# Performance work log

Hardware: AMD Instinct MI355X
Metric: run time of the kernel (lower is better)

## Reference

```python
import jax, jax.numpy as jnp
import numpy as np

# Model dims (match init_kwargs)
H = 2048          # hidden_size
I = 1408          # moe_intermediate_size
E = 16            # n_routed_experts
K = 2             # num_experts_per_tok
N_SHARED = 2      # n_shared_experts -> shared intermediate = I * N_SHARED
IS = I * N_SHARED
ROUTED_SCALE = 1.0
# Expert capacity for the static dispatch buffer. Mean load = T*K/E = 512;
CAPACITY = 1024


def setup_inputs() -> dict:
    key = jax.random.key(0)
    ks = jax.random.split(key, 8)
    B, S = 2, 1024
    scale = 0.02
    return {
        "hidden_states": jax.random.normal(ks[0], (B, S, H), jnp.float32),
        "gate_w": jax.random.normal(ks[1], (E, H), jnp.float32) * scale,      # router logits weight
        "w_gate": jax.random.normal(ks[2], (E, H, I), jnp.float32) * scale,   # expert gate_proj
        "w_up": jax.random.normal(ks[3], (E, H, I), jnp.float32) * scale,     # expert up_proj
        "w_down": jax.random.normal(ks[4], (E, I, H), jnp.float32) * scale,   # expert down_proj
        "ws_gate": jax.random.normal(ks[5], (H, IS), jnp.float32) * scale,    # shared gate_proj
        "ws_up": jax.random.normal(ks[6], (H, IS), jnp.float32) * scale,      # shared up_proj
        "ws_down": jax.random.normal(ks[7], (IS, H), jnp.float32) * scale,    # shared down_proj
    }


def _moe_forward(hidden_states, gate_w, w_gate, w_up, w_down, ws_gate, ws_up, ws_down):
    B, S, _ = hidden_states.shape
    x = hidden_states.reshape(-1, H)                      # [T, H]
    T = x.shape[0]

    # ---- MoEGate: softmax scores, greedy top-k (no renorm, scale=1.0) ----
    logits = jnp.einsum('th,eh->te', x.astype(jnp.float32), gate_w.astype(jnp.float32))
    scores = jax.nn.softmax(logits, axis=-1)              # [T, E]
    topk_w, topk_idx = jax.lax.top_k(scores, K)           # [T, K]
    topk_w = (topk_w * ROUTED_SCALE).astype(x.dtype)

    # ---- dispatch: sort token-assignments by expert (argsort + gather) ----
    flat_idx = topk_idx.reshape(-1)                       # [T*K]
    order = jnp.argsort(flat_idx)                         # stable sort by expert id
    sorted_e = flat_idx[order]                            # expert id per sorted slot
    sorted_t = order // K                                 # source token per sorted slot
    counts = jnp.bincount(flat_idx, length=E)             # tokens per expert
    starts = jnp.cumsum(counts) - counts                  # exclusive prefix sum
    pos = jnp.arange(T * K) - starts[sorted_e]            # slot within its expert group

    # [E, CAPACITY, H] buffer; pos < CAPACITY always holds at this scale
    buf = jnp.zeros((E, CAPACITY, H), x.dtype).at[sorted_e, pos].set(x[sorted_t], mode='drop')

    # ---- per-expert SwiGLU MLP as batched GEMMs over the expert dim ----
    g = jax.nn.silu(jnp.einsum('ech,ehi->eci', buf, w_gate))
    u = jnp.einsum('ech,ehi->eci', buf, w_up)
    expert_out = jnp.einsum('eci,eih->ech', g * u, w_down)  # [E, C, H]

    # ---- combine: gather back, unpermute, weighted sum over k ----
    gathered = expert_out[sorted_e, pos]                  # [T*K, H] in sorted order
    out_flat = jnp.zeros((T * K, H), x.dtype).at[order].set(gathered)
    y = (out_flat.reshape(T, K, H) * topk_w[..., None]).sum(axis=1)  # [T, H]

    # ---- shared experts on the identity path ----
    sh = jnp.einsum('ti,ih->th', jax.nn.silu(x @ ws_gate) * (x @ ws_up), ws_down)
    return (y + sh).reshape(B, S, H)


def reference(hidden_states, gate_w, w_gate, w_up, w_down, ws_gate, ws_up, ws_down):
    return _moe_forward(hidden_states, gate_w, w_gate, w_up, w_down, ws_gate, ws_up, ws_down)
```

## Files before the change

### kernel.cpp

```cpp
#include <hip/hip_runtime.h>
#include <hip/hip_bf16.h>
#include <stdint.h>
#include <math.h>

#define H_DIM 2048
#define I_DIM 1408
#define E_NUM 16
#define IS_DIM 2816
#define T_NUM 2048
#define A_NUM 4096

typedef float f32x4 __attribute__((ext_vector_type(4)));
typedef __bf16 bf16x8 __attribute__((ext_vector_type(8)));
typedef __bf16 bf16x4 __attribute__((ext_vector_type(4)));

__device__ __forceinline__ void async16(const __bf16* g, __bf16* l) {
  __builtin_amdgcn_global_load_lds((__attribute__((address_space(1))) void*)g,
                                   (__attribute__((address_space(3))) void*)l,
                                   16, 0, 0);
}

__global__ __launch_bounds__(256) void k_convert_x(const float* __restrict__ x,
                                                   __bf16* __restrict__ xb) {
  int i = (blockIdx.x * 256 + threadIdx.x) * 4;
  float4 v = *(const float4*)(x + i);
  bf16x4 o;
  o[0] = (__bf16)v.x; o[1] = (__bf16)v.y; o[2] = (__bf16)v.z; o[3] = (__bf16)v.w;
  *(bf16x4*)(xb + i) = o;
}

__global__ __launch_bounds__(256) void k_router(const float* __restrict__ x,
                                                const float* __restrict__ gw,
                                                int* __restrict__ tki,
                                                float* __restrict__ tkw) {
  __shared__ float red[E_NUM * 256];
  __shared__ float st[256];
  __shared__ float sc[E_NUM];
  int t = blockIdx.x, tid = threadIdx.x;
  const float* xr = x + (size_t)t * H_DIM + tid * 8;
  float4 xv0 = *(const float4*)xr;
  float4 xv1 = *(const float4*)(xr + 4);
#pragma unroll
  for (int e = 0; e < E_NUM; e++) {
    const float* g = gw + e * H_DIM + tid * 8;
    float4 a = *(const float4*)g;
    float4 b = *(const float4*)(g + 4);
    red[e * 256 + tid] = xv0.x * a.x + xv0.y * a.y + xv0.z * a.z + xv0.w * a.w +
                         xv1.x * b.x + xv1.y * b.y + xv1.z * b.z + xv1.w * b.w;
  }
  __syncthreads();
  {
    int e = tid >> 4, j = tid & 15;
    float s = 0.f;
#pragma unroll
    for (int m = 0; m < 16; m++) s += red[e * 256 + m * 16 + j];
    st[e * 16 + j] = s;
  }
  __syncthreads();
  if (tid < E_NUM) {
    float s = 0.f;
#pragma unroll
    for (int m = 0; m < 16; m++) s += st[tid * 16 + m];
    sc[tid] = s;
  }
  __syncthreads();
  if (tid == 0) {
    int i1 = 0;
    for (int q = 1; q < E_NUM; q++) if (sc[q] > sc[i1]) i1 = q;
    int i2 = (i1 == 0) ? 1 : 0;
    for (int q = 0; q < E_NUM; q++) if (q != i1 && sc[q] > sc[i2]) i2 = q;
    float mx = sc[i1], Z = 0.f;
    for (int q = 0; q < E_NUM; q++) Z += expf(sc[q] - mx);
    tki[t * 2] = i1;
    tki[t * 2 + 1] = i2;
    tkw[t * 2] = 1.0f / Z;
    tkw[t * 2 + 1] = expf(sc[i2] - mx) / Z;
  }
}

__global__ __launch_bounds__(256) void k_count(const int* __restrict__ tki,
                                               int* __restrict__ grp,
                                               int* __restrict__ cur,
                                               int* __restrict__ grps,
                                               __bf16* __restrict__ zb) {
  __shared__ int cnt[E_NUM];
  int tid = threadIdx.x;
  if (tid < E_NUM) cnt[tid] = 0;
  __syncthreads();
  for (int i = tid; i < A_NUM; i += 256) atomicAdd(&cnt[tki[i]], 1);
  __syncthreads();
  if (tid == 0) {
    int off = 0;
    for (int e = 0; e < E_NUM; e++) { grp[e] = off; cur[e] = off; off += cnt[e]; }
    grp[E_NUM] = off;
    grps[0] = 0; grps[1] = T_NUM;
  }
  if (tid < 64) zb[tid] = (__bf16)0.f;
}

__global__ __launch_bounds__(256) void k_fill(const int* __restrict__ tki,
                                              int* __restrict__ cur,
                                              int* __restrict__ slot_of,
                                              int* __restrict__ tok_of) {
  int i = blockIdx.x * 256 + threadIdx.x;
  if (i < A_NUM) {
    int e = tki[i];
    int s = atomicAdd(&cur[e], 1);
    slot_of[i] = s;
    tok_of[s] = i >> 1;
  }
}

__global__ __launch_bounds__(256) void k_gather(const __bf16* __restrict__ xb,
                                                const int* __restrict__ tok_of,
                                                __bf16* __restrict__ buf) {
  int gid = blockIdx.x * 256 + threadIdx.x;
  int s = gid >> 8;
  int off = (gid & 255) * 8;
  int t = tok_of[s];
  *(uint4*)(buf + (size_t)s * H_DIM + off) = *(const uint4*)(xb + (size_t)t * H_DIM + off);
}

__global__ __launch_bounds__(256) void k_transpose(const float* __restrict__ in,
                                                   __bf16* __restrict__ out,
                                                   int R, int C) {
  __shared__ float tile[32][33];
  size_t zb = (size_t)blockIdx.z * R * C;
  int c0 = blockIdx.x * 32, r0 = blockIdx.y * 32;
  int x = threadIdx.x, y = threadIdx.y;
#pragma unroll
  for (int i = 0; i < 4; i++)
    tile[y + 8 * i][x] = in[zb + (size_t)(r0 + y + 8 * i) * C + c0 + x];
  __syncthreads();
#pragma unroll
  for (int i = 0; i < 4; i++)
    out[zb + (size_t)(c0 + y + 8 * i) * R + r0 + x] = (__bf16)tile[x][y + 8 * i];
}

__global__ __launch_bounds__(256) void k_gemm(const __bf16* __restrict__ A,
                                              const __bf16* __restrict__ Bt,
                                              __bf16* __restrict__ C,
                                              const int* __restrict__ grp,
                                              const __bf16* __restrict__ zb,
                                              int K, int N) {
  int g = blockIdx.z;
  int mstart = grp[g], mend = grp[g + 1];
  int m0 = mstart + blockIdx.y * 128;
  if (m0 >= mend) return;
  int n0 = blockIdx.x * 128;
  const __bf16* Bg = Bt + (size_t)g * N * K;

  __shared__ __align__(16) __bf16 As[128 * 32];
  __shared__ __align__(16) __bf16 Bs[128 * 32];

  int tid = threadIdx.x;
  int wave = tid >> 6, lane = tid & 63;
  int srow = wave * 16 + (lane >> 2);
  int scol = (lane & 3) * 8;

  int rA1 = m0 + srow, rA2 = m0 + srow + 64;
  bool okA1 = rA1 < mend, okA2 = rA2 < mend;
  const __bf16* baseA1 = A + (size_t)rA1 * K + scol;
  const __bf16* baseA2 = A + (size_t)rA2 * K + scol;
  const __bf16* baseB1 = Bg + (size_t)(n0 + srow) * K + scol;
  const __bf16* baseB2 = Bg + (size_t)(n0 + srow + 64) * K + scol;

  __bf16* ldsA1 = As + wave * 512;
  __bf16* ldsA2 = As + 2048 + wave * 512;
  __bf16* ldsB1 = Bs + wave * 512;
  __bf16* ldsB2 = Bs + 2048 + wave * 512;

  int wm = (wave >> 1) * 64, wn = (wave & 1) * 64;
  int r16 = lane & 15, quad = lane >> 4;

  f32x4 acc[4][4] = {};
  for (int k0 = 0; k0 < K; k0 += 32) {
    __syncthreads();
    async16(okA1 ? baseA1 + k0 : zb, ldsA1);
    async16(okA2 ? baseA2 + k0 : zb, ldsA2);
    async16(baseB1 + k0, ldsB1);
    async16(baseB2 + k0, ldsB2);
    __syncthreads();
    bf16x8 af[4], bq[4];
#pragma unroll
    for (int i = 0; i < 4; i++)
      af[i] = *(const bf16x8*)(As + (wm + i * 16 + r16) * 32 + quad * 8);
#pragma unroll
    for (int i = 0; i < 4; i++)
      bq[i] = *(const bf16x8*)(Bs + (wn + i * 16 + r16) * 32 + quad * 8);
#pragma unroll
    for (int mi = 0; mi < 4; mi++)
#pragma unroll
      for (int ni = 0; ni < 4; ni++)
        acc[mi][ni] = __builtin_amdgcn_mfma_f32_16x16x32_bf16(af[mi], bq[ni],
                                                              acc[mi][ni], 0, 0, 0);
  }
#pragma unroll
  for (int mi = 0; mi < 4; mi++) {
    int row_base = m0 + wm + mi * 16 + quad * 4;
#pragma unroll
    for (int r = 0; r < 4; r++) {
      int row = row_base + r;
      if (row < mend) {
#pragma unroll
        for (int ni = 0; ni < 4; ni++) {
          int col = n0 + wn + ni * 16 + r16;
          C[(size_t)row * N + col] = (__bf16)acc[mi][ni][r];
        }
      }
    }
  }
}

__global__ __launch_bounds__(256) void k_silu_mul(const __bf16* __restrict__ G,
                                                  const __bf16* __restrict__ U,
                                                  __bf16* __restrict__ M) {
  int i = (blockIdx.x * 256 + threadIdx.x) * 4;
  bf16x4 g = *(const bf16x4*)(G + i);
  bf16x4 u = *(const bf16x4*)(U + i);
  bf16x4 o;
#pragma unroll
  for (int j = 0; j < 4; j++) {
    float gv = (float)g[j], uv = (float)u[j];
    float s = gv / (1.f + expf(-gv));
    o[j] = (__bf16)(s * uv);
  }
  *(bf16x4*)(M + i) = o;
}

__global__ __launch_bounds__(256) void k_combine(const __bf16* __restrict__ SH,
                                                 const __bf16* __restrict__ EO,
                                                 const int* __restrict__ slot_of,
                                                 const float* __restrict__ tkw,
                                                 float* __restrict__ out) {
  int gid = blockIdx.x * 256 + threadIdx.x;
  int t = gid >> 9;
  int c = (gid & 511) * 4;
  int s1 = slot_of[t * 2], s2 = slot_of[t * 2 + 1];
  float w1 = tkw[t * 2], w2 = tkw[t * 2 + 1];
  bf16x4 sh = *(const bf16x4*)(SH + (size_t)t * H_DIM + c);
  bf16x4 e1 = *(const bf16x4*)(EO + (size_t)s1 * H_DIM + c);
  bf16x4 e2 = *(const bf16x4*)(EO + (size_t)s2 * H_DIM + c);
  float4 o;
  o.x = (float)sh[0] + w1 * (float)e1[0] + w2 * (float)e2[0];
  o.y = (float)sh[1] + w1 * (float)e1[1] + w2 * (float)e2[1];
  o.z = (float)sh[2] + w1 * (float)e1[2] + w2 * (float)e2[2];
  o.w = (float)sh[3] + w1 * (float)e1[3] + w2 * (float)e2[3];
  *(float4*)(out + (size_t)t * H_DIM + c) = o;
}

extern "C" void kernel_launch(void* const* d_in, const int* in_sizes, int n_in,
                              void* d_out, int out_size, void* d_ws, size_t ws_size,
                              hipStream_t stream) {
  const float* x       = (const float*)d_in[0];
  const float* gate_w  = (const float*)d_in[1];
  const float* w_gate  = (const float*)d_in[2];
  const float* w_up    = (const float*)d_in[3];
  const float* w_down  = (const float*)d_in[4];
  const float* ws_gate = (const float*)d_in[5];
  const float* ws_up   = (const float*)d_in[6];
  const float* ws_down = (const float*)d_in[7];
  float* out = (float*)d_out;

  char* p = (char*)d_ws;
  auto alloc = [&](size_t bytes) {
    char* r = p;
    p += (bytes + 255) & ~(size_t)255;
    return r;
  };
  __bf16* WT   = (__bf16*)alloc((size_t)E_NUM * H_DIM * I_DIM * 2);
  __bf16* XB   = (__bf16*)alloc((size_t)T_NUM * H_DIM * 2);
  __bf16* BUF  = (__bf16*)alloc((size_t)A_NUM * H_DIM * 2);
  __bf16* G    = (__bf16*)alloc((size_t)A_NUM * I_DIM * 2);
  __bf16* U    = (__bf16*)alloc((size_t)A_NUM * I_DIM * 2);
  __bf16* M    = (__bf16*)alloc((size_t)A_NUM * I_DIM * 2);
  __bf16* EO   = (__bf16*)alloc((size_t)A_NUM * H_DIM * 2);
  __bf16* SH   = (__bf16*)alloc((size_t)T_NUM * H_DIM * 2);
  int* TKI     = (int*)alloc(A_NUM * 4);
  float* TKW   = (float*)alloc(A_NUM * 4);
  int* GRP     = (int*)alloc(128);
  int* GRPS    = (int*)alloc(128);
  int* CUR     = (int*)alloc(128);
  int* SLOT    = (int*)alloc(A_NUM * 4);
  int* TOK     = (int*)alloc(A_NUM * 4);
  __bf16* ZB   = (__bf16*)alloc(256);
  if ((size_t)(p - (char*)d_ws) > ws_size) return;

  k_convert_x<<<4096, 256, 0, stream>>>(x, XB);
  k_router<<<2048, 256, 0, stream>>>(x, gate_w, TKI, TKW);
  k_count<<<1, 256, 0, stream>>>(TKI, GRP, CUR, GRPS, ZB);
  k_fill<<<16, 256, 0, stream>>>(TKI, CUR, SLOT, TOK);
  k_gather<<<4096, 256, 0, stream>>>(XB, TOK, BUF);

  k_transpose<<<dim3(44, 64, 16), dim3(32, 8), 0, stream>>>(w_gate, WT, 2048, 1408);
  k_gemm<<<dim3(11, 8, 16), 256, 0, stream>>>(BUF, WT, G, GRP, ZB, 2048, 1408);
  k_transpose<<<dim3(44, 64, 16), dim3(32, 8), 0, stream>>>(w_up, WT, 2048, 1408);
  k_gemm<<<dim3(11, 8, 16), 256, 0, stream>>>(BUF, WT, U, GRP, ZB, 2048, 1408);
  k_silu_mul<<<5632, 256, 0, stream>>>(G, U, M);
  k_transpose<<<dim3(64, 44, 16), dim3(32, 8), 0, stream>>>(w_down, WT, 1408, 2048);
  k_gemm<<<dim3(16, 8, 16), 256, 0, stream>>>(M, WT, EO, GRP, ZB, 1408, 2048);

  k_transpose<<<dim3(88, 64, 1), dim3(32, 8), 0, stream>>>(ws_gate, WT, 2048, 2816);
  k_gemm<<<dim3(22, 16, 1), 256, 0, stream>>>(XB, WT, G, GRPS, ZB, 2048, 2816);
  k_transpose<<<dim3(88, 64, 1), dim3(32, 8), 0, stream>>>(ws_up, WT, 2048, 2816);
  k_gemm<<<dim3(22, 16, 1), 256, 0, stream>>>(XB, WT, U, GRPS, ZB, 2048, 2816);
  k_silu_mul<<<5632, 256, 0, stream>>>(G, U, M);
  k_transpose<<<dim3(64, 88, 1), dim3(32, 8), 0, stream>>>(ws_down, WT, 2816, 2048);
  k_gemm<<<dim3(16, 16, 1), 256, 0, stream>>>(M, WT, SH, GRPS, ZB, 2816, 2048);

  k_combine<<<4096, 256, 0, stream>>>(SH, EO, SLOT, TKW, out);
}
```

Before: 1.034 ms.

## Fuse gate/up GEMMs with SiLU epilogue, merge dispatch kernels, enlarge transpose tiles

Gate and up projections are computed in one GEMM kernel that shares the A tile and applies SiLU·up in the epilogue, so the separate G/U buffers and the silu_mul kernel go away. The count and fill kernels are merged into a single dispatch kernel that uses shared-memory atomics. Weight transposes now use 64x64 tiles with a 64x4 thread block. The down GEMM uses 128x64 tiles to give more blocks. Together these cut launches and intermediate HBM traffic, but each block now does less work per A load for the down GEMM, and the transposes use a larger LDS footprint.

```diff
diff --git a/kernel.cpp b/kernel.cpp
--- a/kernel.cpp
+++ b/kernel.cpp
@@ -18,6 +18,10 @@
   __builtin_amdgcn_global_load_lds((__attribute__((address_space(1))) void*)g,
                                    (__attribute__((address_space(3))) void*)l,
                                    16, 0, 0);
+}
+
+__device__ __forceinline__ float silu_f(float g) {
+  return g / (1.f + __expf(-g));
 }
 
 __global__ __launch_bounds__(256) void k_convert_x(const float* __restrict__ x,
@@ -78,12 +82,14 @@
   }
 }
 
-__global__ __launch_bounds__(256) void k_count(const int* __restrict__ tki,
-                                               int* __restrict__ grp,
-                                               int* __restrict__ cur,
-                                               int* __restrict__ grps,
-                                               __bf16* __restrict__ zb) {
+__global__ __launch_bounds__(256) void k_dispatch(const int* __restrict__ tki,
+                                                  int* __restrict__ grp,
+                                                  int* __restrict__ grps,
+                                                  int* __restrict__ slot_of,
+                                                  int* __restrict__ tok_of,
+                                                  __bf16* __restrict__ zb) {
   __shared__ int cnt[E_NUM];
+  __shared__ int cur[E_NUM];
   int tid = threadIdx.x;
   if (tid < E_NUM) cnt[tid] = 0;
   __syncthreads();
@@ -96,14 +102,8 @@
     grps[0] = 0; grps[1] = T_NUM;
   }
   if (tid < 64) zb[tid] = (__bf16)0.f;
-}
-
-__global__ __launch_bounds__(256) void k_fill(const int* __restrict__ tki,
-                                              int* __restrict__ cur,
-                                              int* __restrict__ slot_of,
-                                              int* __restrict__ tok_of) {
-  int i = blockIdx.x * 256 + threadIdx.x;
-  if (i < A_NUM) {
+  __syncthreads();
+  for (int i = tid; i < A_NUM; i += 256) {
     int e = tki[i];
     int s = atomicAdd(&cur[e], 1);
     slot_of[i] = s;
@@ -124,34 +124,37 @@
 __global__ __launch_bounds__(256) void k_transpose(const float* __restrict__ in,
                                                    __bf16* __restrict__ out,
                                                    int R, int C) {
-  __shared__ float tile[32][33];
+  __shared__ float tile[64][65];
   size_t zb = (size_t)blockIdx.z * R * C;
-  int c0 = blockIdx.x * 32, r0 = blockIdx.y * 32;
+  int c0 = blockIdx.x * 64, r0 = blockIdx.y * 64;
   int x = threadIdx.x, y = threadIdx.y;
 #pragma unroll
-  for (int i = 0; i < 4; i++)
-    tile[y + 8 * i][x] = in[zb + (size_t)(r0 + y + 8 * i) * C + c0 + x];
-  __syncthreads();
-#pragma unroll
-  for (int i = 0; i < 4; i++)
-    out[zb + (size_t)(c0 + y + 8 * i) * R + r0 + x] = (__bf16)tile[x][y + 8 * i];
-}
-
-__global__ __launch_bounds__(256) void k_gemm(const __bf16* __restrict__ A,
-                                              const __bf16* __restrict__ Bt,
-                                              __bf16* __restrict__ C,
-                                              const int* __restrict__ grp,
-                                              const __bf16* __restrict__ zb,
-                                              int K, int N) {
+  for (int i = 0; i < 16; i++)
+    tile[y + 4 * i][x] = in[zb + (size_t)(r0 + y + 4 * i) * C + c0 + x];
+  __syncthreads();
+#pragma unroll
+  for (int i = 0; i < 16; i++)
+    out[zb + (size_t)(c0 + y + 4 * i) * R + r0 + x] = (__bf16)tile[x][y + 4 * i];
+}
+
+__global__ __launch_bounds__(256) void k_gemm_gu(const __bf16* __restrict__ A,
+                                                 const __bf16* __restrict__ Bg,
+                                                 const __bf16* __restrict__ Bu,
+                                                 __bf16* __restrict__ Mb,
+                                                 const int* __restrict__ grp,
+                                                 const __bf16* __restrict__ zb,
+                                                 int K, int N) {
   int g = blockIdx.z;
   int mstart = grp[g], mend = grp[g + 1];
   int m0 = mstart + blockIdx.y * 128;
   if (m0 >= mend) return;
-  int n0 = blockIdx.x * 128;
-  const __bf16* Bg = Bt + (size_t)g * N * K;
+  int n0 = blockIdx.x * 64;
+  const __bf16* Bgg = Bg + (size_t)g * N * K;
+  const __bf16* Bug = Bu + (size_t)g * N * K;
 
   __shared__ __align__(16) __bf16 As[128 * 32];
-  __shared__ __align__(16) __bf16 Bs[128 * 32];
+  __shared__ __align__(16) __bf16 Gs[64 * 32];
+  __shared__ __align__(16) __bf16 Us[64 * 32];
 
   int tid = threadIdx.x;
   int wave = tid >> 6, lane = tid & 63;
@@ -162,38 +165,43 @@
   bool okA1 = rA1 < mend, okA2 = rA2 < mend;
   const __bf16* baseA1 = A + (size_t)rA1 * K + scol;
   const __bf16* baseA2 = A + (size_t)rA2 * K + scol;
-  const __bf16* baseB1 = Bg + (size_t)(n0 + srow) * K + scol;
-  const __bf16* baseB2 = Bg + (size_t)(n0 + srow + 64) * K + scol;
+  const __bf16* baseG = Bgg + (size_t)(n0 + srow) * K + scol;
+  const __bf16* baseU = Bug + (size_t)(n0 + srow) * K + scol;
 
   __bf16* ldsA1 = As + wave * 512;
   __bf16* ldsA2 = As + 2048 + wave * 512;
-  __bf16* ldsB1 = Bs + wave * 512;
-  __bf16* ldsB2 = Bs + 2048 + wave * 512;
-
-  int wm = (wave >> 1) * 64, wn = (wave & 1) * 64;
+  __bf16* ldsG = Gs + wave * 512;
+  __bf16* ldsU = Us + wave * 512;
+
+  int wm = (wave >> 1) * 64, wn = (wave & 1) * 32;
   int r16 = lane & 15, quad = lane >> 4;
 
-  f32x4 acc[4][4] = {};
+  f32x4 accg[4][2] = {}, accu[4][2] = {};
   for (int k0 = 0; k0 < K; k0 += 32) {
     __syncthreads();
     async16(okA1 ? baseA1 + k0 : zb, ldsA1);
     async16(okA2 ? baseA2 + k0 : zb, ldsA2);
-    async16(baseB1 + k0, ldsB1);
-    async16(baseB2 + k0, ldsB2);
+    async16(baseG + k0, ldsG);
+    async16(baseU + k0, ldsU);
     __syncthreads();
-    bf16x8 af[4], bq[4];
+    bf16x8 af[4], bg[2], bu[2];
 #pragma unroll
     for (int i = 0; i < 4; i++)
       af[i] = *(const bf16x8*)(As + (wm + i * 16 + r16) * 32 + quad * 8);
 #pragma unroll
-    for (int i = 0; i < 4; i++)
-      bq[i] = *(const bf16x8*)(Bs + (wn + i * 16 + r16) * 32 + quad * 8);
+    for (int i = 0; i < 2; i++) {
+      bg[i] = *(const bf16x8*)(Gs + (wn + i * 16 + r16) * 32 + quad * 8);
+      bu[i] = *(const bf16x8*)(Us + (wn + i * 16 + r16) * 32 + quad * 8);
+    }
 #pragma unroll
     for (int mi = 0; mi < 4; mi++)
 #pragma unroll
-      for (int ni = 0; ni < 4; ni++)
-        acc[mi][ni] = __builtin_amdgcn_mfma_f32_16x16x32_bf16(af[mi], bq[ni],
-                                                              acc[mi][ni], 0, 0, 0);
+      for (int ni = 0; ni < 2; ni++) {
+        accg[mi][ni] = __builtin_amdgcn_mfma_f32_16x16x32_bf16(af[mi], bg[ni],
+                                                               accg[mi][ni], 0, 0, 0);
+        accu[mi][ni] = __builtin_amdgcn_mfma_f32_16x16x32_bf16(af[mi], bu[ni],
+                                                               accu[mi][ni], 0, 0, 0);
+      }
   }
 #pragma unroll
   for (int mi = 0; mi < 4; mi++) {
@@ -203,29 +211,86 @@
       int row = row_base + r;
       if (row < mend) {
 #pragma unroll
-        for (int ni = 0; ni < 4; ni++) {
+        for (int ni = 0; ni < 2; ni++) {
+          int col = n0 + wn + ni * 16 + r16;
+          float v = silu_f(accg[mi][ni][r]) * accu[mi][ni][r];
+          Mb[(size_t)row * N + col] = (__bf16)v;
+        }
+      }
+    }
+  }
+}
+
+__global__ __launch_bounds__(256) void k_gemm_dn(const __bf16* __restrict__ A,
+                                                 const __bf16* __restrict__ Bt,
+                                                 __bf16* __restrict__ C,
+                                                 const int* __restrict__ grp,
+                                                 const __bf16* __restrict__ zb,
+                                                 int K, int N) {
+  int g = blockIdx.z;
+  int mstart = grp[g], mend = grp[g + 1];
+  int m0 = mstart + blockIdx.y * 128;
+  if (m0 >= mend) return;
+  int n0 = blockIdx.x * 64;
+  const __bf16* Bg = Bt + (size_t)g * N * K;
+
+  __shared__ __align__(16) __bf16 As[128 * 32];
+  __shared__ __align__(16) __bf16 Bs[64 * 32];
+
+  int tid = threadIdx.x;
+  int wave = tid >> 6, lane = tid & 63;
+  int srow = wave * 16 + (lane >> 2);
+  int scol = (lane & 3) * 8;
+
+  int rA1 = m0 + srow, rA2 = m0 + srow + 64;
+  bool okA1 = rA1 < mend, okA2 = rA2 < mend;
+  const __bf16* baseA1 = A + (size_t)rA1 * K + scol;
+  const __bf16* baseA2 = A + (size_t)rA2 * K + scol;
+  const __bf16* baseB = Bg + (size_t)(n0 + srow) * K + scol;
+
+  __bf16* ldsA1 = As + wave * 512;
+  __bf16* ldsA2 = As + 2048 + wave * 512;
+  __bf16* ldsB = Bs + wave * 512;
+
+  int wm = (wave >> 1) * 64, wn = (wave & 1) * 32;
+  int r16 = lane & 15, quad = lane >> 4;
+
+  f32x4 acc[4][2] = {};
+  for (int k0 = 0; k0 < K; k0 += 32) {
+    __syncthreads();
+    async16(okA1 ? baseA1 + k0 : zb, ldsA1);
+    async16(okA2 ? baseA2 + k0 : zb, ldsA2);
+    async16(baseB + k0, ldsB);
+    __syncthreads();
+    bf16x8 af[4], bq[2];
+#pragma unroll
+    for (int i = 0; i < 4; i++)
+      af[i] = *(const bf16x8*)(As + (wm + i * 16 + r16) * 32 + quad * 8);
+#pragma unroll
+    for (int i = 0; i < 2; i++)
+      bq[i] = *(const bf16x8*)(Bs + (wn + i * 16 + r16) * 32 + quad * 8);
+#pragma unroll
+    for (int mi = 0; mi < 4; mi++)
+#pragma unroll
+      for (int ni = 0; ni < 2; ni++)
+        acc[mi][ni] = __builtin_amdgcn_mfma_f32_16x16x32_bf16(af[mi], bq[ni],
+                                                              acc[mi][ni], 0, 0, 0);
+  }
+#pragma unroll
+  for (int mi = 0; mi < 4; mi++) {
+    int row_base = m0 + wm + mi * 16 + quad * 4;
+#pragma unroll
+    for (int r = 0; r < 4; r++) {
+      int row = row_base + r;
+      if (row < mend) {
+#pragma unroll
+        for (int ni = 0; ni < 2; ni++) {
           int col = n0 + wn + ni * 16 + r16;
           C[(size_t)row * N + col] = (__bf16)acc[mi][ni][r];
         }
       }
     }
   }
-}
-
-__global__ __launch_bounds__(256) void k_silu_mul(const __bf16* __restrict__ G,
-                                                  const __bf16* __restrict__ U,
-                                                  __bf16* __restrict__ M) {
-  int i = (blockIdx.x * 256 + threadIdx.x) * 4;
-  bf16x4 g = *(const bf16x4*)(G + i);
-  bf16x4 u = *(const bf16x4*)(U + i);
-  bf16x4 o;
-#pragma unroll
-  for (int j = 0; j < 4; j++) {
-    float gv = (float)g[j], uv = (float)u[j];
-    float s = gv / (1.f + expf(-gv));
-    o[j] = (__bf16)(s * uv);
-  }
-  *(bf16x4*)(M + i) = o;
 }
 
 __global__ __launch_bounds__(256) void k_combine(const __bf16* __restrict__ SH,
@@ -268,19 +333,17 @@
     p += (bytes + 255) & ~(size_t)255;
     return r;
   };
-  __bf16* WT   = (__bf16*)alloc((size_t)E_NUM * H_DIM * I_DIM * 2);
+  __bf16* WT1  = (__bf16*)alloc((size_t)E_NUM * H_DIM * I_DIM * 2);
+  __bf16* WT2  = (__bf16*)alloc((size_t)E_NUM * H_DIM * I_DIM * 2);
   __bf16* XB   = (__bf16*)alloc((size_t)T_NUM * H_DIM * 2);
   __bf16* BUF  = (__bf16*)alloc((size_t)A_NUM * H_DIM * 2);
-  __bf16* G    = (__bf16*)alloc((size_t)A_NUM * I_DIM * 2);
-  __bf16* U    = (__bf16*)alloc((size_t)A_NUM * I_DIM * 2);
-  __bf16* M    = (__bf16*)alloc((size_t)A_NUM * I_DIM * 2);
+  __bf16* Mb   = (__bf16*)alloc((size_t)A_NUM * I_DIM * 2);
   __bf16* EO   = (__bf16*)alloc((size_t)A_NUM * H_DIM * 2);
   __bf16* SH   = (__bf16*)alloc((size_t)T_NUM * H_DIM * 2);
   int* TKI     = (int*)alloc(A_NUM * 4);
   float* TKW   = (float*)alloc(A_NUM * 4);
   int* GRP     = (int*)alloc(128);
   int* GRPS    = (int*)alloc(128);
-  int* CUR     = (int*)alloc(128);
   int* SLOT    = (int*)alloc(A_NUM * 4);
   int* TOK     = (int*)alloc(A_NUM * 4);
   __bf16* ZB   = (__bf16*)alloc(256);
@@ -288,25 +351,20 @@
 
   k_convert_x<<<4096, 256, 0, stream>>>(x, XB);
   k_router<<<2048, 256, 0, stream>>>(x, gate_w, TKI, TKW);
-  k_count<<<1, 256, 0, stream>>>(TKI, GRP, CUR, GRPS, ZB);
-  k_fill<<<16, 256, 0, stream>>>(TKI, CUR, SLOT, TOK);
+  k_dispatch<<<1, 256, 0, stream>>>(TKI, GRP, GRPS, SLOT, TOK, ZB);
   k_gather<<<4096, 256, 0, stream>>>(XB, TOK, BUF);
 
-  k_transpose<<<dim3(44, 64, 16), dim3(32, 8), 0, stream>>>(w_gate, WT, 2048, 1408);
-  k_gemm<<<dim3(11, 8, 16), 256, 0, stream>>>(BUF, WT, G, GRP, ZB, 2048, 1408);
-  k_transpose<<<dim3(44, 64, 16), dim3(32, 8), 0, stream>>>(w_up, WT, 2048, 1408);
-  k_gemm<<<dim3(11, 8, 16), 256, 0, stream>>>(BUF, WT, U, GRP, ZB, 2048, 1408);
-  k_silu_mul<<<5632, 256, 0, stream>>>(G, U, M);
-  k_transpose<<<dim3(64, 44, 16), dim3(32, 8), 0, stream>>>(w_down, WT, 1408, 2048);
-  k_gemm<<<dim3(16, 8, 16), 256, 0, stream>>>(M, WT, EO, GRP, ZB, 1408, 2048);
-
-  k_transpose<<<dim3(88, 64, 1), dim3(32, 8), 0, stream>>>(ws_gate, WT, 2048, 2816);
-  k_gemm<<<dim3(22, 16, 1), 256, 0, stream>>>(XB, WT, G, GRPS, ZB, 2048, 2816);
-  k_transpose<<<dim3(88, 64, 1), dim3(32, 8), 0, stream>>>(ws_up, WT, 2048, 2816);
-  k_gemm<<<dim3(22, 16, 1), 256, 0, stream>>>(XB, WT, U, GRPS, ZB, 2048, 2816);
-  k_silu_mul<<<5632, 256, 0, stream>>>(G, U, M);
-  k_transpose<<<dim3(64, 88, 1), dim3(32, 8), 0, stream>>>(ws_down, WT, 2816, 2048);
-  k_gemm<<<dim3(16, 16, 1), 256, 0, stream>>>(M, WT, SH, GRPS, ZB, 2816, 2048);
+  k_transpose<<<dim3(22, 32, 16), dim3(64, 4), 0, stream>>>(w_gate, WT1, 2048, 1408);
+  k_transpose<<<dim3(22, 32, 16), dim3(64, 4), 0, stream>>>(w_up, WT2, 2048, 1408);
+  k_gemm_gu<<<dim3(22, 8, 16), 256, 0, stream>>>(BUF, WT1, WT2, Mb, GRP, ZB, 2048, 1408);
+  k_transpose<<<dim3(32, 22, 16), dim3(64, 4), 0, stream>>>(w_down, WT1, 1408, 2048);
+  k_gemm_dn<<<dim3(32, 8, 16), 256, 0, stream>>>(Mb, WT1, EO, GRP, ZB, 1408, 2048);
+
+  k_transpose<<<dim3(44, 32, 1), dim3(64, 4), 0, stream>>>(ws_gate, WT1, 2048, 2816);
+  k_transpose<<<dim3(44, 32, 1), dim3(64, 4), 0, stream>>>(ws_up, WT2, 2048, 2816);
+  k_gemm_gu<<<dim3(44, 16, 1), 256, 0, stream>>>(XB, WT1, WT2, Mb, GRPS, ZB, 2048, 2816);
+  k_transpose<<<dim3(32, 44, 1), dim3(64, 4), 0, stream>>>(ws_down, WT1, 2816, 2048);
+  k_gemm_dn<<<dim3(32, 16, 1), 256, 0, stream>>>(Mb, WT1, SH, GRPS, ZB, 2816, 2048);
 
   k_combine<<<4096, 256, 0, stream>>>(SH, EO, SLOT, TKW, out);
 }
```

Measured after the change: 933.5 us. 1.11x faster.
